# Optimization experiments

Measured on AMD Instinct MI355X. Metric: run time of the kernel, lower is better.

Reference implementation:

```python
import jax, jax.numpy as jnp
import numpy as np

# Intersection(mode='product'):
#   a_fk = a @ feats.T            # [Na, K]
#   b_fk = b @ feats.T            # [Nb, K]
#   mask = (a_fk[:,None,:] > 0) & (b_fk[None,:,:] > 0)
#   result = sum_k (a_fk[:,None,:] * b_fk[None,:,:]) * mask   # [Na, Nb]
# For the product op, (x*y)*[x>0 & y>0] == relu(x)*relu(y) elementwise
# (any term with a non-positive factor is zeroed either way), so the
# broadcast+mask+reduce collapses exactly into a GEMM over relu'd scores.

def setup_inputs() -> dict:
    key = jax.random.key(0)
    k1, k2, k3 = jax.random.split(key, 3)
    a = jax.random.normal(k1, (1024, 2048), dtype=jnp.float32)
    b = jax.random.normal(k2, (1024, 2048), dtype=jnp.float32)
    feats = jax.random.normal(k3, (128, 2048), dtype=jnp.float32)
    return {"a": a, "b": b, "feats": feats}

def reference(a, b, feats):
    a_fk = a @ feats.T            # [Na, K]
    b_fk = b @ feats.T            # [Nb, K]
    # masked product-intersection reduced over K; identical math to the
    # broadcast (Na, Nb, K) -> sum formulation of the torch module.
    return jnp.einsum('ak,bk->ab', jax.nn.relu(a_fk), jax.nn.relu(b_fk))
```

## Files before the change

### kernel.cpp

```cpp
#include <hip/hip_runtime.h>


typedef __attribute__((ext_vector_type(8))) __bf16 bf16x8;
typedef __attribute__((ext_vector_type(4))) float floatx4;

#define KD   2048
#define NF   128
#define NA   1024

static __device__ inline bf16x8 cvt8(float4 u, float4 v) {
    bf16x8 s;
    s[0] = (__bf16)u.x; s[1] = (__bf16)u.y; s[2] = (__bf16)u.z; s[3] = (__bf16)u.w;
    s[4] = (__bf16)v.x; s[5] = (__bf16)v.y; s[6] = (__bf16)v.z; s[7] = (__bf16)v.w;
    return s;
}

static __device__ inline bf16x8 cvt8_relu(float4 u, float4 v) {
    bf16x8 s;
    s[0] = (__bf16)fmaxf(u.x, 0.f); s[1] = (__bf16)fmaxf(u.y, 0.f);
    s[2] = (__bf16)fmaxf(u.z, 0.f); s[3] = (__bf16)fmaxf(u.w, 0.f);
    s[4] = (__bf16)fmaxf(v.x, 0.f); s[5] = (__bf16)fmaxf(v.y, 0.f);
    s[6] = (__bf16)fmaxf(v.z, 0.f); s[7] = (__bf16)fmaxf(v.w, 0.f);
    return s;
}

__global__ __launch_bounds__(256) void zero_fk(float* __restrict__ fk) {
    int i = blockIdx.x * 256 + threadIdx.x;
    ((float4*)fk)[i] = make_float4(0.f, 0.f, 0.f, 0.f);
}

__global__ __launch_bounds__(256) void gemm1(const float* __restrict__ A,
                                             const float* __restrict__ B,
                                             const float* __restrict__ F,
                                             float* __restrict__ fk) {
    __shared__ __bf16 Xs[64 * 40];
    __shared__ __bf16 Fs[128 * 40];

    const int t    = threadIdx.x;
    const int m0   = blockIdx.x * 64;
    const int k0   = blockIdx.y * 256;
    const float* src = (m0 < NA) ? (A + (size_t)m0 * KD)
                                 : (B + (size_t)(m0 - NA) * KD);

    const int lane = t & 63;
    const int w    = t >> 6;
    const int ln   = lane & 15;
    const int quad = lane >> 4;
    const int q8   = quad * 8;

    floatx4 acc[4][2];
#pragma unroll
    for (int mt = 0; mt < 4; mt++)
#pragma unroll
        for (int nt = 0; nt < 2; nt++)
            acc[mt][nt] = (floatx4){0.f, 0.f, 0.f, 0.f};

    const int xrow = t >> 2, xcol = (t & 3) * 8;
    const int frow = t >> 1, fcol = (t & 1) * 16;

    for (int kk = 0; kk < 256; kk += 32) {
        {
            const float* p = src + (size_t)xrow * KD + (k0 + kk + xcol);
            float4 u = *(const float4*)p;
            float4 v = *(const float4*)(p + 4);
            *(bf16x8*)&Xs[xrow * 40 + xcol] = cvt8(u, v);
        }
        {
            const float* p = F + (size_t)frow * KD + (k0 + kk + fcol);
            float4 u0 = *(const float4*)(p + 0);
            float4 u1 = *(const float4*)(p + 4);
            float4 u2 = *(const float4*)(p + 8);
            float4 u3 = *(const float4*)(p + 12);
            *(bf16x8*)&Fs[frow * 40 + fcol]     = cvt8(u0, u1);
            *(bf16x8*)&Fs[frow * 40 + fcol + 8] = cvt8(u2, u3);
        }
        __syncthreads();

        bf16x8 bfrag[2];
#pragma unroll
        for (int nt = 0; nt < 2; nt++)
            bfrag[nt] = *(const bf16x8*)&Fs[(w * 32 + nt * 16 + ln) * 40 + q8];
#pragma unroll
        for (int mt = 0; mt < 4; mt++) {
            bf16x8 af = *(const bf16x8*)&Xs[(mt * 16 + ln) * 40 + q8];
#pragma unroll
            for (int nt = 0; nt < 2; nt++)
                acc[mt][nt] = __builtin_amdgcn_mfma_f32_16x16x32_bf16(
                    af, bfrag[nt], acc[mt][nt], 0, 0, 0);
        }
        __syncthreads();
    }

#pragma unroll
    for (int mt = 0; mt < 4; mt++)
#pragma unroll
        for (int nt = 0; nt < 2; nt++)
#pragma unroll
            for (int r = 0; r < 4; r++) {
                int row = m0 + mt * 16 + quad * 4 + r;
                int col = w * 32 + nt * 16 + ln;
                atomicAdd(&fk[row * NF + col], acc[mt][nt][r]);
            }
}

__global__ __launch_bounds__(256) void gemm2(const float* __restrict__ fk,
                                             float* __restrict__ out) {
    __shared__ __bf16 Ps[64 * 136];
    __shared__ __bf16 Qs[64 * 136];

    const int t    = threadIdx.x;
    const int i0   = blockIdx.y * 64;
    const int j0   = blockIdx.x * 64;
    const int lane = t & 63;
    const int w    = t >> 6;
    const int wm   = w & 1;
    const int wn   = w >> 1;
    const int ln   = lane & 15;
    const int quad = lane >> 4;
    const int q8   = quad * 8;

    const int prow = t >> 2, pcol = (t & 3) * 32;
    {
        const float* p = fk + (size_t)(i0 + prow) * NF + pcol;
        const float* q = fk + (size_t)(NA + j0 + prow) * NF + pcol;
#pragma unroll
        for (int c = 0; c < 32; c += 8) {
            float4 u = *(const float4*)(p + c);
            float4 v = *(const float4*)(p + c + 4);
            *(bf16x8*)&Ps[prow * 136 + pcol + c] = cvt8_relu(u, v);
            float4 x = *(const float4*)(q + c);
            float4 y = *(const float4*)(q + c + 4);
            *(bf16x8*)&Qs[prow * 136 + pcol + c] = cvt8_relu(x, y);
        }
    }
    __syncthreads();

    floatx4 acc[2][2];
#pragma unroll
    for (int mt = 0; mt < 2; mt++)
#pragma unroll
        for (int nt = 0; nt < 2; nt++)
            acc[mt][nt] = (floatx4){0.f, 0.f, 0.f, 0.f};

#pragma unroll
    for (int k0 = 0; k0 < 128; k0 += 32) {
        bf16x8 af[2], bf[2];
#pragma unroll
        for (int mt = 0; mt < 2; mt++)
            af[mt] = *(const bf16x8*)&Ps[(wm * 32 + mt * 16 + ln) * 136 + k0 + q8];
#pragma unroll
        for (int nt = 0; nt < 2; nt++)
            bf[nt] = *(const bf16x8*)&Qs[(wn * 32 + nt * 16 + ln) * 136 + k0 + q8];
#pragma unroll
        for (int mt = 0; mt < 2; mt++)
#pragma unroll
            for (int nt = 0; nt < 2; nt++)
                acc[mt][nt] = __builtin_amdgcn_mfma_f32_16x16x32_bf16(
                    af[mt], bf[nt], acc[mt][nt], 0, 0, 0);
    }

#pragma unroll
    for (int mt = 0; mt < 2; mt++)
#pragma unroll
        for (int nt = 0; nt < 2; nt++)
#pragma unroll
            for (int r = 0; r < 4; r++) {
                int row = i0 + wm * 32 + mt * 16 + quad * 4 + r;
                int col = j0 + wn * 32 + nt * 16 + ln;
                out[(size_t)row * 1024 + col] = acc[mt][nt][r];
            }
}

extern "C" void kernel_launch(void* const* d_in, const int* in_sizes, int n_in,
                              void* d_out, int out_size, void* d_ws, size_t ws_size,
                              hipStream_t stream) {
    const float* a     = (const float*)d_in[0];
    const float* b     = (const float*)d_in[1];
    const float* feats = (const float*)d_in[2];
    float* out = (float*)d_out;
    float* fk  = (float*)d_ws;

    zero_fk<<<256, 256, 0, stream>>>(fk);
    gemm1<<<dim3(32, 8), 256, 0, stream>>>(a, b, feats, fk);
    gemm2<<<dim3(16, 16), 256, 0, stream>>>(fk, out);
}
```

Baseline: 85.15 us.

## Replace atomic split-K accumulation with partial buffers and a relu-reduce kernel

```diff
diff --git a/kernel.cpp b/kernel.cpp
--- a/kernel.cpp
+++ b/kernel.cpp
@@ -2,11 +2,14 @@
 
 
 typedef __attribute__((ext_vector_type(8))) __bf16 bf16x8;
+typedef __attribute__((ext_vector_type(4))) __bf16 bf16x4;
 typedef __attribute__((ext_vector_type(4))) float floatx4;
 
-#define KD   2048
-#define NF   128
-#define NA   1024
+#define KD     2048
+#define NF     128
+#define NA     1024
+#define NPART  16
+#define FKN    (2048 * 128)
 
 static __device__ inline bf16x8 cvt8(float4 u, float4 v) {
     bf16x8 s;
@@ -15,30 +18,17 @@
     return s;
 }
 
-static __device__ inline bf16x8 cvt8_relu(float4 u, float4 v) {
-    bf16x8 s;
-    s[0] = (__bf16)fmaxf(u.x, 0.f); s[1] = (__bf16)fmaxf(u.y, 0.f);
-    s[2] = (__bf16)fmaxf(u.z, 0.f); s[3] = (__bf16)fmaxf(u.w, 0.f);
-    s[4] = (__bf16)fmaxf(v.x, 0.f); s[5] = (__bf16)fmaxf(v.y, 0.f);
-    s[6] = (__bf16)fmaxf(v.z, 0.f); s[7] = (__bf16)fmaxf(v.w, 0.f);
-    return s;
-}
-
-__global__ __launch_bounds__(256) void zero_fk(float* __restrict__ fk) {
-    int i = blockIdx.x * 256 + threadIdx.x;
-    ((float4*)fk)[i] = make_float4(0.f, 0.f, 0.f, 0.f);
-}
-
-__global__ __launch_bounds__(256) void gemm1(const float* __restrict__ A,
-                                             const float* __restrict__ B,
-                                             const float* __restrict__ F,
-                                             float* __restrict__ fk) {
+__global__ __launch_bounds__(256) void gemm1_part(const float* __restrict__ A,
+                                                  const float* __restrict__ B,
+                                                  const float* __restrict__ F,
+                                                  float* __restrict__ part) {
     __shared__ __bf16 Xs[64 * 40];
     __shared__ __bf16 Fs[128 * 40];
 
     const int t    = threadIdx.x;
     const int m0   = blockIdx.x * 64;
-    const int k0   = blockIdx.y * 256;
+    const int s    = blockIdx.y;
+    const int k0   = s * 128;
     const float* src = (m0 < NA) ? (A + (size_t)m0 * KD)
                                  : (B + (size_t)(m0 - NA) * KD);
 
@@ -58,7 +48,8 @@
     const int xrow = t >> 2, xcol = (t & 3) * 8;
     const int frow = t >> 1, fcol = (t & 1) * 16;
 
-    for (int kk = 0; kk < 256; kk += 32) {
+#pragma unroll
+    for (int kk = 0; kk < 128; kk += 32) {
         {
             const float* p = src + (size_t)xrow * KD + (k0 + kk + xcol);
             float4 u = *(const float4*)p;
@@ -91,6 +82,7 @@
         __syncthreads();
     }
 
+    float* pdst = part + (size_t)s * FKN;
 #pragma unroll
     for (int mt = 0; mt < 4; mt++)
 #pragma unroll
@@ -99,11 +91,29 @@
             for (int r = 0; r < 4; r++) {
                 int row = m0 + mt * 16 + quad * 4 + r;
                 int col = w * 32 + nt * 16 + ln;
-                atomicAdd(&fk[row * NF + col], acc[mt][nt][r]);
+                pdst[(size_t)row * NF + col] = acc[mt][nt][r];
             }
 }
 
-__global__ __launch_bounds__(256) void gemm2(const float* __restrict__ fk,
+__global__ __launch_bounds__(256) void reduce_relu(const float* __restrict__ part,
+                                                   __bf16* __restrict__ fkb) {
+    int idx = blockIdx.x * 256 + threadIdx.x;
+    size_t base = (size_t)idx * 4;
+    float4 sum = make_float4(0.f, 0.f, 0.f, 0.f);
+#pragma unroll
+    for (int s = 0; s < NPART; s++) {
+        float4 u = *(const float4*)(part + (size_t)s * FKN + base);
+        sum.x += u.x; sum.y += u.y; sum.z += u.z; sum.w += u.w;
+    }
+    bf16x4 o;
+    o[0] = (__bf16)fmaxf(sum.x, 0.f);
+    o[1] = (__bf16)fmaxf(sum.y, 0.f);
+    o[2] = (__bf16)fmaxf(sum.z, 0.f);
+    o[3] = (__bf16)fmaxf(sum.w, 0.f);
+    *(bf16x4*)(fkb + base) = o;
+}
+
+__global__ __launch_bounds__(256) void gemm2(const __bf16* __restrict__ fkb,
                                              float* __restrict__ out) {
     __shared__ __bf16 Ps[64 * 136];
     __shared__ __bf16 Qs[64 * 136];
@@ -121,16 +131,12 @@
 
     const int prow = t >> 2, pcol = (t & 3) * 32;
     {
-        const float* p = fk + (size_t)(i0 + prow) * NF + pcol;
-        const float* q = fk + (size_t)(NA + j0 + prow) * NF + pcol;
+        const __bf16* p = fkb + (size_t)(i0 + prow) * NF + pcol;
+        const __bf16* q = fkb + (size_t)(NA + j0 + prow) * NF + pcol;
 #pragma unroll
         for (int c = 0; c < 32; c += 8) {
-            float4 u = *(const float4*)(p + c);
-            float4 v = *(const float4*)(p + c + 4);
-            *(bf16x8*)&Ps[prow * 136 + pcol + c] = cvt8_relu(u, v);
-            float4 x = *(const float4*)(q + c);
-            float4 y = *(const float4*)(q + c + 4);
-            *(bf16x8*)&Qs[prow * 136 + pcol + c] = cvt8_relu(x, y);
+            *(bf16x8*)&Ps[prow * 136 + pcol + c] = *(const bf16x8*)(p + c);
+            *(bf16x8*)&Qs[prow * 136 + pcol + c] = *(const bf16x8*)(q + c);
         }
     }
     __syncthreads();
@@ -178,9 +184,11 @@
     const float* b     = (const float*)d_in[1];
     const float* feats = (const float*)d_in[2];
     float* out = (float*)d_out;
-    float* fk  = (float*)d_ws;
 
-    zero_fk<<<256, 256, 0, stream>>>(fk);
-    gemm1<<<dim3(32, 8), 256, 0, stream>>>(a, b, feats, fk);
-    gemm2<<<dim3(16, 16), 256, 0, stream>>>(fk, out);
+    float*   part = (float*)d_ws;
+    __bf16*  fkb  = (__bf16*)((char*)d_ws + (size_t)NPART * FKN * 4);
+
+    gemm1_part<<<dim3(32, NPART), 256, 0, stream>>>(a, b, feats, part);
+    reduce_relu<<<256, 256, 0, stream>>>(part, fkb);
+    gemm2<<<dim3(16, 16), 256, 0, stream>>>(fkb, out);
 }
```

Measured after the change: 79.36 us. 6.8% less time.

## Replace atomic split-K reduction with partial buffers summed in second GEMM

Applied to the files above, without the earlier changes.

```diff
diff --git a/kernel.cpp b/kernel.cpp
--- a/kernel.cpp
+++ b/kernel.cpp
@@ -4,9 +4,13 @@
 typedef __attribute__((ext_vector_type(8))) __bf16 bf16x8;
 typedef __attribute__((ext_vector_type(4))) float floatx4;
 
-#define KD   2048
-#define NF   128
-#define NA   1024
+#define KD     2048
+#define NF     128
+#define NA     1024
+#define NSPLIT 8
+#define KSP    256
+#define BK     128
+#define FKN    (2048 * 128)
 
 static __device__ inline bf16x8 cvt8(float4 u, float4 v) {
     bf16x8 s;
@@ -14,7 +18,6 @@
     s[4] = (__bf16)v.x; s[5] = (__bf16)v.y; s[6] = (__bf16)v.z; s[7] = (__bf16)v.w;
     return s;
 }
-
 static __device__ inline bf16x8 cvt8_relu(float4 u, float4 v) {
     bf16x8 s;
     s[0] = (__bf16)fmaxf(u.x, 0.f); s[1] = (__bf16)fmaxf(u.y, 0.f);
@@ -23,87 +26,95 @@
     s[6] = (__bf16)fmaxf(v.z, 0.f); s[7] = (__bf16)fmaxf(v.w, 0.f);
     return s;
 }
-
-__global__ __launch_bounds__(256) void zero_fk(float* __restrict__ fk) {
-    int i = blockIdx.x * 256 + threadIdx.x;
-    ((float4*)fk)[i] = make_float4(0.f, 0.f, 0.f, 0.f);
+static __device__ inline void acc4(float4& d, float4 u) {
+    d.x += u.x; d.y += u.y; d.z += u.z; d.w += u.w;
 }
 
 __global__ __launch_bounds__(256) void gemm1(const float* __restrict__ A,
                                              const float* __restrict__ B,
                                              const float* __restrict__ F,
-                                             float* __restrict__ fk) {
-    __shared__ __bf16 Xs[64 * 40];
-    __shared__ __bf16 Fs[128 * 40];
+                                             float* __restrict__ part) {
+    __shared__ __bf16 Xs[32 * 136];
+    __shared__ __bf16 Fs[128 * 136];
 
     const int t    = threadIdx.x;
-    const int m0   = blockIdx.x * 64;
-    const int k0   = blockIdx.y * 256;
-    const float* src = (m0 < NA) ? (A + (size_t)m0 * KD)
-                                 : (B + (size_t)(m0 - NA) * KD);
-
     const int lane = t & 63;
     const int w    = t >> 6;
     const int ln   = lane & 15;
     const int quad = lane >> 4;
     const int q8   = quad * 8;
 
-    floatx4 acc[4][2];
-#pragma unroll
-    for (int mt = 0; mt < 4; mt++)
+    const int m0 = blockIdx.x * 32;
+    const int s  = blockIdx.y;
+    const int k0 = s * KSP;
+    const float* src = (m0 < NA) ? (A + (size_t)m0 * KD)
+                                 : (B + (size_t)(m0 - NA) * KD);
+
+    floatx4 acc[2][2];
+#pragma unroll
+    for (int mt = 0; mt < 2; mt++)
 #pragma unroll
         for (int nt = 0; nt < 2; nt++)
             acc[mt][nt] = (floatx4){0.f, 0.f, 0.f, 0.f};
 
-    const int xrow = t >> 2, xcol = (t & 3) * 8;
-    const int frow = t >> 1, fcol = (t & 1) * 16;
-
-    for (int kk = 0; kk < 256; kk += 32) {
+    const int xr = t >> 3, xc = (t & 7) * 16;
+    const int fr = t >> 1, fc = (t & 1) * 64;
+
+#pragma unroll
+    for (int kk = 0; kk < KSP; kk += BK) {
         {
-            const float* p = src + (size_t)xrow * KD + (k0 + kk + xcol);
-            float4 u = *(const float4*)p;
-            float4 v = *(const float4*)(p + 4);
-            *(bf16x8*)&Xs[xrow * 40 + xcol] = cvt8(u, v);
-        }
-        {
-            const float* p = F + (size_t)frow * KD + (k0 + kk + fcol);
+            const float* p = src + (size_t)xr * KD + (k0 + kk + xc);
             float4 u0 = *(const float4*)(p + 0);
             float4 u1 = *(const float4*)(p + 4);
             float4 u2 = *(const float4*)(p + 8);
             float4 u3 = *(const float4*)(p + 12);
-            *(bf16x8*)&Fs[frow * 40 + fcol]     = cvt8(u0, u1);
-            *(bf16x8*)&Fs[frow * 40 + fcol + 8] = cvt8(u2, u3);
+            *(bf16x8*)&Xs[xr * 136 + xc]     = cvt8(u0, u1);
+            *(bf16x8*)&Xs[xr * 136 + xc + 8] = cvt8(u2, u3);
+        }
+        {
+            const float* p = F + (size_t)fr * KD + (k0 + kk + fc);
+#pragma unroll
+            for (int j = 0; j < 64; j += 16) {
+                float4 u0 = *(const float4*)(p + j + 0);
+                float4 u1 = *(const float4*)(p + j + 4);
+                float4 u2 = *(const float4*)(p + j + 8);
+                float4 u3 = *(const float4*)(p + j + 12);
+                *(bf16x8*)&Fs[fr * 136 + fc + j]     = cvt8(u0, u1);
+                *(bf16x8*)&Fs[fr * 136 + fc + j + 8] = cvt8(u2, u3);
+            }
         }
         __syncthreads();
 
-        bf16x8 bfrag[2];
-#pragma unroll
-        for (int nt = 0; nt < 2; nt++)
-            bfrag[nt] = *(const bf16x8*)&Fs[(w * 32 + nt * 16 + ln) * 40 + q8];
-#pragma unroll
-        for (int mt = 0; mt < 4; mt++) {
-            bf16x8 af = *(const bf16x8*)&Xs[(mt * 16 + ln) * 40 + q8];
+#pragma unroll
+        for (int ks = 0; ks < BK; ks += 32) {
+            bf16x8 bfrag[2];
 #pragma unroll
             for (int nt = 0; nt < 2; nt++)
-                acc[mt][nt] = __builtin_amdgcn_mfma_f32_16x16x32_bf16(
-                    af, bfrag[nt], acc[mt][nt], 0, 0, 0);
+                bfrag[nt] = *(const bf16x8*)&Fs[(w * 32 + nt * 16 + ln) * 136 + ks + q8];
+#pragma unroll
+            for (int mt = 0; mt < 2; mt++) {
+                bf16x8 af = *(const bf16x8*)&Xs[(mt * 16 + ln) * 136 + ks + q8];
+#pragma unroll
+                for (int nt = 0; nt < 2; nt++)
+                    acc[mt][nt] = __builtin_amdgcn_mfma_f32_16x16x32_bf16(
+                        af, bfrag[nt], acc[mt][nt], 0, 0, 0);
+            }
         }
         __syncthreads();
     }
 
-#pragma unroll
-    for (int mt = 0; mt < 4; mt++)
-#pragma unroll
-        for (int nt = 0; nt < 2; nt++)
-#pragma unroll
-            for (int r = 0; r < 4; r++) {
-                int row = m0 + mt * 16 + quad * 4 + r;
-                int col = w * 32 + nt * 16 + ln;
-                atomicAdd(&fk[row * NF + col], acc[mt][nt][r]);
-            }
-}
-
-__global__ __launch_bounds__(256) void gemm2(const float* __restrict__ fk,
+    float* pdst = part + (size_t)s * FKN;
+#pragma unroll
+    for (int mt = 0; mt < 2; mt++)
+#pragma unroll
+        for (int nt = 0; nt < 2; nt++)
+#pragma unroll
+            for (int r = 0; r < 4; r++)
+                pdst[(size_t)(m0 + mt * 16 + quad * 4 + r) * NF
+                     + (w * 32 + nt * 16 + ln)] = acc[mt][nt][r];
+}
+
+__global__ __launch_bounds__(256) void gemm2(const float* __restrict__ part,
                                              float* __restrict__ out) {
     __shared__ __bf16 Ps[64 * 136];
     __shared__ __bf16 Qs[64 * 136];
@@ -121,16 +132,23 @@
 
     const int prow = t >> 2, pcol = (t & 3) * 32;
     {
-        const float* p = fk + (size_t)(i0 + prow) * NF + pcol;
-        const float* q = fk + (size_t)(NA + j0 + prow) * NF + pcol;
+        const size_t pbase = (size_t)(i0 + prow) * NF + pcol;
+        const size_t qbase = (size_t)(NA + j0 + prow) * NF + pcol;
 #pragma unroll
         for (int c = 0; c < 32; c += 8) {
-            float4 u = *(const float4*)(p + c);
-            float4 v = *(const float4*)(p + c + 4);
-            *(bf16x8*)&Ps[prow * 136 + pcol + c] = cvt8_relu(u, v);
-            float4 x = *(const float4*)(q + c);
-            float4 y = *(const float4*)(q + c + 4);
-            *(bf16x8*)&Qs[prow * 136 + pcol + c] = cvt8_relu(x, y);
+            float4 p0 = make_float4(0.f, 0.f, 0.f, 0.f), p1 = p0;
+            float4 q0 = p0, q1 = p0;
+#pragma unroll
+            for (int s = 0; s < NSPLIT; s++) {
+                const float* pp = part + (size_t)s * FKN + pbase + c;
+                const float* qq = part + (size_t)s * FKN + qbase + c;
+                acc4(p0, *(const float4*)(pp + 0));
+                acc4(p1, *(const float4*)(pp + 4));
+                acc4(q0, *(const float4*)(qq + 0));
+                acc4(q1, *(const float4*)(qq + 4));
+            }
+            *(bf16x8*)&Ps[prow * 136 + pcol + c] = cvt8_relu(p0, p1);
+            *(bf16x8*)&Qs[prow * 136 + pcol + c] = cvt8_relu(q0, q1);
         }
     }
     __syncthreads();
@@ -143,7 +161,7 @@
             acc[mt][nt] = (floatx4){0.f, 0.f, 0.f, 0.f};
 
 #pragma unroll
-    for (int k0 = 0; k0 < 128; k0 += 32) {
+    for (int k0 = 0; k0 < NF; k0 += 32) {
         bf16x8 af[2], bf[2];
 #pragma unroll
         for (int mt = 0; mt < 2; mt++)
@@ -177,10 +195,9 @@
     const float* a     = (const float*)d_in[0];
     const float* b     = (const float*)d_in[1];
     const float* feats = (const float*)d_in[2];
-    float* out = (float*)d_out;
-    float* fk  = (float*)d_ws;
-
-    zero_fk<<<256, 256, 0, stream>>>(fk);
-    gemm1<<<dim3(32, 8), 256, 0, stream>>>(a, b, feats, fk);
-    gemm2<<<dim3(16, 16), 256, 0, stream>>>(fk, out);
-}
+    float* out  = (float*)d_out;
+    float* part = (float*)d_ws;
+
+    gemm1<<<dim3(64, NSPLIT), 256, 0, stream>>>(a, b, feats, part);
+    gemm2<<<dim3(16, 16), 256, 0, stream>>>(part, out);
+}
```

After: 105.2 us. 23.5% more time.
